# Kernel optimization log

Hardware: AMD Instinct MI355X
Metric: run time of the kernel (lower is better)

The kernel has to match this reference:

```python
import jax, jax.numpy as jnp
import numpy as np


def log_g(x):
    # log of g(x) = relu(x)+0.5 for x>=0, sigmoid(x) for x<0 (continuous minGRU activation)
    return jnp.where(x >= 0, jnp.log(jax.nn.relu(x) + 0.5), -jax.nn.softplus(-x))


def parallel_scan_log(log_coeffs, log_values):
    # log_coeffs: [B,T,H], log_values: [B,T+1,H]
    a_star = jnp.pad(jnp.cumsum(log_coeffs, axis=1), ((0, 0), (1, 0), (0, 0)))  # [B,T+1,H]
    log_h = a_star + jax.lax.cumlogsumexp(log_values - a_star, axis=1)
    return jnp.exp(log_h)  # [B,T+1,H]


def setup_inputs() -> dict:
    key = jax.random.key(0)
    B, T, D, H = 8, 4096, 1024, 1024
    k1, k2, k3, k4, k5, k6 = jax.random.split(key, 6)
    scale = 1.0 / np.sqrt(D)
    return {
        "x": jax.random.normal(k1, (B, T, D), dtype=jnp.float32),
        "h_0": jax.random.uniform(k2, (B, 1, H), dtype=jnp.float32),
        "W_z": jax.random.uniform(k3, (H, D), minval=-scale, maxval=scale, dtype=jnp.float32),
        "b_z": jax.random.uniform(k4, (H,), minval=-scale, maxval=scale, dtype=jnp.float32),
        "W_h": jax.random.uniform(k5, (H, D), minval=-scale, maxval=scale, dtype=jnp.float32),
        "b_h": jax.random.uniform(k6, (H,), minval=-scale, maxval=scale, dtype=jnp.float32),
    }


def reference(x, h_0, W_z, b_z, W_h, b_h):
    # k = linear_z(x)
    k = jnp.einsum('btd,hd->bth', x, W_z) + b_z                 # [B,T,H]
    log_z = -jax.nn.softplus(-k)                                # log sigmoid(k)
    log_coeffs = -jax.nn.softplus(k)                            # log (1 - sigmoid(k))
    log_h_0 = log_g(h_0)                                        # [B,1,H]
    log_tilde_h = log_g(jnp.einsum('btd,hd->bth', x, W_h) + b_h)  # [B,T,H]
    log_values = jnp.concatenate([log_h_0, log_z + log_tilde_h], axis=1)  # [B,T+1,H]
    h = parallel_scan_log(log_coeffs, log_values)               # [B,T+1,H]
    return h
```

## Files before the change

kernel.cpp:

```cpp
#include <hip/hip_runtime.h>
#include <stdint.h>

#define B_ 8
#define T_ 4096
#define D_ 1024
#define H_ 1024
#define M_ (B_*T_)
#define K_ D_
#define N_ H_
#define TC 32
#define NC (T_/TC)

typedef short short8 __attribute__((ext_vector_type(8)));
typedef float f32x4 __attribute__((ext_vector_type(4)));
typedef unsigned short ushort8v __attribute__((ext_vector_type(8)));

__device__ __forceinline__ float bf2f(unsigned short u) {
    union { unsigned int i; float f; } x; x.i = ((unsigned int)u) << 16; return x.f;
}
__device__ __forceinline__ unsigned short f2bf(float f) {
    union { float f; unsigned int i; } x; x.f = f;
    unsigned int u = x.i;
    unsigned int r = u + 0x7fffu + ((u >> 16) & 1u);
    return (unsigned short)(r >> 16);
}
__device__ __forceinline__ void gld_lds16(const unsigned short* g, unsigned short* l) {
    __builtin_amdgcn_global_load_lds(
        (const __attribute__((address_space(1))) void*)(const void*)g,
        (__attribute__((address_space(3))) void*)(void*)l, 16, 0, 0);
}
__device__ __forceinline__ float sigm_neg(float k) {
    return __builtin_amdgcn_rcpf(1.f + __expf(k));
}
__device__ __forceinline__ float gfun(float x) {
    float neg = __builtin_amdgcn_rcpf(1.f + __expf(-x));
    return x >= 0.f ? x + 0.5f : neg;
}

__global__ void cvt_kernel(const float* __restrict__ src, unsigned short* __restrict__ dst, int n4) {
    int i = blockIdx.x * blockDim.x + threadIdx.x;
    const int stride = gridDim.x * blockDim.x;
    for (; i < n4; i += stride) {
        float4 v = ((const float4*)src)[i];
        ushort4 o;
        o.x = f2bf(v.x); o.y = f2bf(v.y); o.z = f2bf(v.z); o.w = f2bf(v.w);
        ((ushort4*)dst)[i] = o;
    }
}

__global__ void cvtw_kernel(const float* __restrict__ Wz, const float* __restrict__ Wh,
                            unsigned short* __restrict__ wzb, unsigned short* __restrict__ whb, int n4) {
    const float* src = blockIdx.y ? Wh : Wz;
    unsigned short* dst = blockIdx.y ? whb : wzb;
    int i = blockIdx.x * blockDim.x + threadIdx.x;
    const int stride = gridDim.x * blockDim.x;
    for (; i < n4; i += stride) {
        float4 v = ((const float4*)src)[i];
        ushort4 o;
        o.x = f2bf(v.x); o.y = f2bf(v.y); o.z = f2bf(v.z); o.w = f2bf(v.w);
        ((ushort4*)dst)[i] = o;
    }
}

#define SB() __builtin_amdgcn_sched_barrier(0)
#define BAR() do { SB(); __builtin_amdgcn_s_barrier(); SB(); } while (0)

__global__ __launch_bounds__(512, 2) void gemm_kernel(
    const unsigned short* __restrict__ Xb,
    const unsigned short* __restrict__ Wzb,
    const unsigned short* __restrict__ Whb,
    const float* __restrict__ bz, const float* __restrict__ bh,
    unsigned short* __restrict__ KzOut, unsigned short* __restrict__ KhOut,
    int row_off)
{
    __shared__ __align__(16) unsigned short ldsA[2][256 * 64];
    __shared__ __align__(16) unsigned short ldsB[2][256 * 64];

    const int bx = blockIdx.x;
    const int bn = blockIdx.y;
    const int mat = blockIdx.z;
    const unsigned short* Wb = mat ? Whb : Wzb;
    const float* bias = mat ? bh : bz;
    unsigned short* Out = mat ? KhOut : KzOut;

    const int tid = threadIdx.x;
    const int w = tid >> 6, lane = tid & 63;
    const int wm = w >> 2, wn = w & 3;

    const int srow = lane >> 3;
    const int schunk = ((lane & 7) ^ srow) << 3;
    const unsigned short* gA = Xb + (size_t)(row_off + bx * 512 + srow) * K_ + schunk;
    const unsigned short* gB = Wb + (size_t)(bn * 256 + srow) * K_ + schunk;

#define STAGE_A(s, g, h) do { \
    gld_lds16(gA + (size_t)(((g) >> 4) * 256 + (h)*128 + w*8) * K_ + ((g)&15) * 64, \
              &ldsA[s][((h)*128 + w*8) * 64]); \
    gld_lds16(gA + (size_t)(((g) >> 4) * 256 + (h)*128 + 64 + w*8) * K_ + ((g)&15) * 64, \
              &ldsA[s][((h)*128 + 64 + w*8) * 64]); \
  } while (0)
#define STAGE_B(s, g, h) do { \
    gld_lds16(gB + (size_t)((h)*128 + w*8) * K_ + ((g)&15) * 64, \
              &ldsB[s][((h)*128 + w*8) * 64]); \
    gld_lds16(gB + (size_t)((h)*128 + 64 + w*8) * K_ + ((g)&15) * 64, \
              &ldsB[s][((h)*128 + 64 + w*8) * 64]); \
  } while (0)

    const int lrow = lane & 15;
    const int q = lane >> 4;
    const int sw0 = (q ^ (lane & 7)) << 3;

#define LDA(s, fm, kh) (*(const short8*)&ldsA[s][(wm*128 + (fm)*16 + lrow) * 64 + (sw0 ^ ((kh)*32))])
#define LDB(s, fn, kh) (*(const short8*)&ldsB[s][(wn*64  + (fn)*16 + lrow) * 64 + (sw0 ^ ((kh)*32))])

#define RD_A4(s, fmb) do { \
    _Pragma("unroll") for (int f = 0; f < 4; ++f) { Ar[f][0] = LDA(s, (fmb)+f, 0); Ar[f][1] = LDA(s, (fmb)+f, 1); } \
  } while (0)
#define RD_B2(s, fnb) do { \
    _Pragma("unroll") for (int g2_ = 0; g2_ < 2; ++g2_) { Br[(fnb)+g2_][0] = LDB(s, (fnb)+g2_, 0); Br[(fnb)+g2_][1] = LDB(s, (fnb)+g2_, 1); } \
  } while (0)

#define QUAD(mb, nb) do { \
    __builtin_amdgcn_s_setprio(1); \
    _Pragma("unroll") for (int f = 0; f < 4; ++f) { \
      _Pragma("unroll") for (int g2_ = 0; g2_ < 2; ++g2_) { \
        acc[(mb)+f][(nb)+g2_] = __builtin_amdgcn_mfma_f32_16x16x32_bf16(Ar[f][0], Br[(nb)+g2_][0], acc[(mb)+f][(nb)+g2_], 0, 0, 0); \
        acc[(mb)+f][(nb)+g2_] = __builtin_amdgcn_mfma_f32_16x16x32_bf16(Ar[f][1], Br[(nb)+g2_][1], acc[(mb)+f][(nb)+g2_], 0, 0, 0); \
      } \
    } \
    __builtin_amdgcn_s_setprio(0); \
  } while (0)

    f32x4 acc[8][4];
    short8 Ar[4][2], Br[4][2];

    float bb[4];
#pragma unroll
    for (int fn = 0; fn < 4; ++fn) bb[fn] = bias[bn * 256 + wn * 64 + fn * 16 + lrow];

    STAGE_B(0, 0, 0); STAGE_B(0, 0, 1);
    STAGE_A(0, 0, 0); STAGE_A(0, 0, 1);
    STAGE_B(1, 1, 0); STAGE_B(1, 1, 1);
    SB();
    asm volatile("s_waitcnt vmcnt(4)" ::: "memory");
    BAR();

#pragma unroll 1
    for (int t = 0; t < 2; ++t) {
#pragma unroll
        for (int i = 0; i < 8; ++i)
#pragma unroll
            for (int j = 0; j < 4; ++j) acc[i][j] = (f32x4){0.f, 0.f, 0.f, 0.f};

#pragma unroll 1
        for (int i = 0; i < 8; ++i) {
            const int g1 = t * 16 + 2 * i + 1;
            const int g2 = g1 + 1;
            const int g3 = g1 + 2;
            const bool st = (g2 < 32);

            RD_A4(0, 0); RD_B2(0, 0);
            STAGE_A(1, g1, 0);
            BAR();
            QUAD(0, 0);
            BAR();
            RD_B2(0, 2);
            STAGE_A(1, g1, 1);
            BAR();
            QUAD(0, 2);
            BAR();
            RD_A4(0, 4);
            if (st) STAGE_B(0, g2, 0);
            BAR();
            QUAD(4, 0);
            BAR();
            if (st) {
                STAGE_B(0, g2, 1);
                SB();
                asm volatile("s_waitcnt vmcnt(4)" ::: "memory");
            } else {
                asm volatile("s_waitcnt vmcnt(0)" ::: "memory");
            }
            BAR();
            QUAD(4, 2);
            BAR();
            RD_A4(1, 0); RD_B2(1, 0);
            if (st) STAGE_A(0, g2, 0);
            BAR();
            QUAD(0, 0);
            BAR();
            RD_B2(1, 2);
            if (st) STAGE_A(0, g2, 1);
            BAR();
            QUAD(0, 2);
            BAR();
            RD_A4(1, 4);
            if (st) STAGE_B(1, g3, 0);
            BAR();
            QUAD(4, 0);
            BAR();
            if (st) {
                STAGE_B(1, g3, 1);
                SB();
                asm volatile("s_waitcnt vmcnt(4)" ::: "memory");
            }
            BAR();
            QUAD(4, 2);
            BAR();
        }

#pragma unroll
        for (int fn = 0; fn < 4; ++fn) {
            const int n = bn * 256 + wn * 64 + fn * 16 + lrow;
#pragma unroll
            for (int fm = 0; fm < 8; ++fm) {
                const int mq = (row_off >> 2) + bx * 128 + t * 64 + wm * 32 + fm * 4 + q;
                ushort4 o;
                o.x = f2bf(acc[fm][fn][0] + bb[fn]);
                o.y = f2bf(acc[fm][fn][1] + bb[fn]);
                o.z = f2bf(acc[fm][fn][2] + bb[fn]);
                o.w = f2bf(acc[fm][fn][3] + bb[fn]);
                *(ushort4*)(Out + ((size_t)mq * N_ + n) * 4) = o;
            }
        }
    }
}


#define QUAD_MATH(Z0, Z1, HH0, HH1, CYSTMT)                                            \
    _Pragma("unroll")                                                                  \
    for (int r = 0; r < 4; r++) {                                                      \
        float kzf[4] = {bf2f(Z0[r]), bf2f(Z0[4 + r]), bf2f(Z1[r]), bf2f(Z1[4 + r])};   \
        float khf[4] = {bf2f(HH0[r]), bf2f(HH0[4 + r]), bf2f(HH1[r]), bf2f(HH1[4 + r])};\
        _Pragma("unroll")                                                              \
        for (int j = 0; j < 4; j++) {                                                  \
            float f = sigm_neg(kzf[j]);                           \
            float v = (1.f - f) * gfun(khf[j]);                 \
            CYSTMT                                                                     \
        }                                                                              \
    }

__global__ __launch_bounds__(256) void scanA_kernel(const unsigned short* __restrict__ Kz,
                                                    const unsigned short* __restrict__ Kh,
                                                    float* __restrict__ Fc, float* __restrict__ Vc)
{
    const int c = blockIdx.x, b = blockIdx.y;
    const int hb = threadIdx.x * 4;
    float F[4] = {1.f, 1.f, 1.f, 1.f}, V[4] = {0.f, 0.f, 0.f, 0.f};
    const size_t base0 = ((size_t)(b * (T_ / 4) + c * (TC / 4)) * N_ + hb) * 4;
    const size_t str = (size_t)N_ * 4;
    ushort8v cz0 = *(const ushort8v*)(Kz + base0);
    ushort8v cz1 = *(const ushort8v*)(Kz + base0 + 8);
    ushort8v ch0 = *(const ushort8v*)(Kh + base0);
    ushort8v ch1 = *(const ushort8v*)(Kh + base0 + 8);
    ushort8v az0 = *(const ushort8v*)(Kz + base0 + str);
    ushort8v az1 = *(const ushort8v*)(Kz + base0 + str + 8);
    ushort8v ah0 = *(const ushort8v*)(Kh + base0 + str);
    ushort8v ah1 = *(const ushort8v*)(Kh + base0 + str + 8);
#pragma unroll 1
    for (int qq = 0; qq < TC / 4; qq++) {
        const int qn = (qq + 2 < TC / 4) ? qq + 2 : TC / 4 - 1;
        const size_t nb = base0 + (size_t)qn * str;
        ushort8v bz0 = *(const ushort8v*)(Kz + nb);
        ushort8v bz1 = *(const ushort8v*)(Kz + nb + 8);
        ushort8v bh0 = *(const ushort8v*)(Kh + nb);
        ushort8v bh1 = *(const ushort8v*)(Kh + nb + 8);
        QUAD_MATH(cz0, cz1, ch0, ch1, { V[j] = f * V[j] + v; F[j] *= f; })
        cz0 = az0; cz1 = az1; ch0 = ah0; ch1 = ah1;
        az0 = bz0; az1 = bz1; ah0 = bh0; ah1 = bh1;
    }
    size_t o = ((size_t)(b * NC + c)) * H_ + hb;
    *(float4*)(Fc + o) = make_float4(F[0], F[1], F[2], F[3]);
    *(float4*)(Vc + o) = make_float4(V[0], V[1], V[2], V[3]);
}

__global__ __launch_bounds__(64) void scanB_kernel(const float* __restrict__ h0,
                                                   const float* __restrict__ Fc,
                                                   const float* __restrict__ Vc,
                                                   float* __restrict__ Carry,
                                                   float* __restrict__ Out)
{
    const int b = blockIdx.x;
    const int h = blockIdx.y * 256 + threadIdx.x * 4;
    float cy[4];
#pragma unroll
    for (int j = 0; j < 4; j++) cy[j] = gfun(h0[(size_t)b * H_ + h + j]);
    *(float4*)(Out + (size_t)b * (T_ + 1) * H_ + h) = make_float4(cy[0], cy[1], cy[2], cy[3]);
    size_t o = ((size_t)(b * NC)) * H_ + h;
    float4 F4 = *(const float4*)(Fc + o);
    float4 V4 = *(const float4*)(Vc + o);
    for (int c = 0; c < NC; c++) {
        const size_t on = o + H_;
        float4 nF, nV;
        if (c + 1 < NC) {
            nF = *(const float4*)(Fc + on);
            nV = *(const float4*)(Vc + on);
        }
        *(float4*)(Carry + o) = make_float4(cy[0], cy[1], cy[2], cy[3]);
        cy[0] = F4.x * cy[0] + V4.x;
        cy[1] = F4.y * cy[1] + V4.y;
        cy[2] = F4.z * cy[2] + V4.z;
        cy[3] = F4.w * cy[3] + V4.w;
        F4 = nF; V4 = nV; o = on;
    }
}

__global__ __launch_bounds__(256) void scanC_kernel(const unsigned short* __restrict__ Kz,
                                                    const unsigned short* __restrict__ Kh,
                                                    const float* __restrict__ Carry,
                                                    float* __restrict__ Out)
{
    const int c = blockIdx.x, b = blockIdx.y;
    const int hb = threadIdx.x * 4;
    float cy[4];
    {
        float4 c4 = *(const float4*)(Carry + ((size_t)(b * NC + c)) * H_ + hb);
        cy[0] = c4.x; cy[1] = c4.y; cy[2] = c4.z; cy[3] = c4.w;
    }
    const size_t base0 = ((size_t)(b * (T_ / 4) + c * (TC / 4)) * N_ + hb) * 4;
    const size_t str = (size_t)N_ * 4;
    size_t ob = ((size_t)(b * (T_ + 1) + c * TC + 1)) * H_ + hb;
    ushort8v cz0 = *(const ushort8v*)(Kz + base0);
    ushort8v cz1 = *(const ushort8v*)(Kz + base0 + 8);
    ushort8v ch0 = *(const ushort8v*)(Kh + base0);
    ushort8v ch1 = *(const ushort8v*)(Kh + base0 + 8);
    ushort8v az0 = *(const ushort8v*)(Kz + base0 + str);
    ushort8v az1 = *(const ushort8v*)(Kz + base0 + str + 8);
    ushort8v ah0 = *(const ushort8v*)(Kh + base0 + str);
    ushort8v ah1 = *(const ushort8v*)(Kh + base0 + str + 8);
#pragma unroll 1
    for (int qq = 0; qq < TC / 4; qq++) {
        const int qn = (qq + 2 < TC / 4) ? qq + 2 : TC / 4 - 1;
        const size_t nb = base0 + (size_t)qn * str;
        ushort8v bz0 = *(const ushort8v*)(Kz + nb);
        ushort8v bz1 = *(const ushort8v*)(Kz + nb + 8);
        ushort8v bh0 = *(const ushort8v*)(Kh + nb);
        ushort8v bh1 = *(const ushort8v*)(Kh + nb + 8);
        QUAD_MATH(cz0, cz1, ch0, ch1, {
            cy[j] = f * cy[j] + v;
            if (j == 3) { *(float4*)(Out + ob) = make_float4(cy[0], cy[1], cy[2], cy[3]); ob += H_; }
        })
        cz0 = az0; cz1 = az1; ch0 = ah0; ch1 = ah1;
        az0 = bz0; az1 = bz1; ah0 = bh0; ah1 = bh1;
    }
}

extern "C" void kernel_launch(void* const* d_in, const int* in_sizes, int n_in,
                              void* d_out, int out_size, void* d_ws, size_t ws_size,
                              hipStream_t stream)
{
    const float* x  = (const float*)d_in[0];
    const float* h0 = (const float*)d_in[1];
    const float* Wz = (const float*)d_in[2];
    const float* bz = (const float*)d_in[3];
    const float* Wh = (const float*)d_in[4];
    const float* bh = (const float*)d_in[5];
    float* out = (float*)d_out;

    char* ws = (char*)d_ws;
    unsigned short* xb  = (unsigned short*)ws; ws += (size_t)M_ * K_ * 2;
    unsigned short* wzb = (unsigned short*)ws; ws += (size_t)N_ * K_ * 2;
    unsigned short* whb = (unsigned short*)ws; ws += (size_t)N_ * K_ * 2;
    unsigned short* kz  = (unsigned short*)ws; ws += (size_t)M_ * N_ * 2;
    unsigned short* kh  = (unsigned short*)ws; ws += (size_t)M_ * N_ * 2;
    float* Fc    = (float*)ws; ws += (size_t)B_ * NC * H_ * 4;
    float* Vc    = (float*)ws; ws += (size_t)B_ * NC * H_ * 4;
    float* Carry = (float*)ws; ws += (size_t)B_ * NC * H_ * 4;

    cvt_kernel<<<2048, 256, 0, stream>>>(x, xb, M_ * K_ / 4);
    cvtw_kernel<<<dim3(128, 2), 256, 0, stream>>>(Wz, Wh, wzb, whb, N_ * K_ / 4);

    dim3 gg(32, 4, 2);
    gemm_kernel<<<gg, 512, 0, stream>>>(xb, wzb, whb, bz, bh, kz, kh, 0);
    gemm_kernel<<<gg, 512, 0, stream>>>(xb, wzb, whb, bz, bh, kz, kh, 16384);

    scanA_kernel<<<dim3(NC, B_), 256, 0, stream>>>(kz, kh, Fc, Vc);
    scanB_kernel<<<dim3(B_, H_ / 256), 64, 0, stream>>>(h0, Fc, Vc, Carry, out);
    scanC_kernel<<<dim3(NC, B_), 256, 0, stream>>>(kz, kh, Carry, out);
}
```

Measured before the change: 450.1 us.

## Merge GEMM launches and prefetch next A fragments during MFMA quads

Result: slower. 465.7 us (+3.5%).

```diff
diff --git a/kernel.cpp b/kernel.cpp
--- a/kernel.cpp
+++ b/kernel.cpp
@@ -70,8 +70,7 @@
     const unsigned short* __restrict__ Wzb,
     const unsigned short* __restrict__ Whb,
     const float* __restrict__ bz, const float* __restrict__ bh,
-    unsigned short* __restrict__ KzOut, unsigned short* __restrict__ KhOut,
-    int row_off)
+    unsigned short* __restrict__ KzOut, unsigned short* __restrict__ KhOut)
 {
     __shared__ __align__(16) unsigned short ldsA[2][256 * 64];
     __shared__ __align__(16) unsigned short ldsB[2][256 * 64];
@@ -89,7 +88,7 @@
 
     const int srow = lane >> 3;
     const int schunk = ((lane & 7) ^ srow) << 3;
-    const unsigned short* gA = Xb + (size_t)(row_off + bx * 512 + srow) * K_ + schunk;
+    const unsigned short* gA = Xb + (size_t)(bx * 1024 + srow) * K_ + schunk;
     const unsigned short* gB = Wb + (size_t)(bn * 256 + srow) * K_ + schunk;
 
 #define STAGE_A(s, g, h) do { \
@@ -112,26 +111,26 @@
 #define LDA(s, fm, kh) (*(const short8*)&ldsA[s][(wm*128 + (fm)*16 + lrow) * 64 + (sw0 ^ ((kh)*32))])
 #define LDB(s, fn, kh) (*(const short8*)&ldsB[s][(wn*64  + (fn)*16 + lrow) * 64 + (sw0 ^ ((kh)*32))])
 
-#define RD_A4(s, fmb) do { \
-    _Pragma("unroll") for (int f = 0; f < 4; ++f) { Ar[f][0] = LDA(s, (fmb)+f, 0); Ar[f][1] = LDA(s, (fmb)+f, 1); } \
+#define RD_A4(DST, s, fmb) do { \
+    _Pragma("unroll") for (int f = 0; f < 4; ++f) { DST[f][0] = LDA(s, (fmb)+f, 0); DST[f][1] = LDA(s, (fmb)+f, 1); } \
   } while (0)
 #define RD_B2(s, fnb) do { \
     _Pragma("unroll") for (int g2_ = 0; g2_ < 2; ++g2_) { Br[(fnb)+g2_][0] = LDB(s, (fnb)+g2_, 0); Br[(fnb)+g2_][1] = LDB(s, (fnb)+g2_, 1); } \
   } while (0)
 
-#define QUAD(mb, nb) do { \
+#define QUAD(AF, mb, nb) do { \
     __builtin_amdgcn_s_setprio(1); \
     _Pragma("unroll") for (int f = 0; f < 4; ++f) { \
       _Pragma("unroll") for (int g2_ = 0; g2_ < 2; ++g2_) { \
-        acc[(mb)+f][(nb)+g2_] = __builtin_amdgcn_mfma_f32_16x16x32_bf16(Ar[f][0], Br[(nb)+g2_][0], acc[(mb)+f][(nb)+g2_], 0, 0, 0); \
-        acc[(mb)+f][(nb)+g2_] = __builtin_amdgcn_mfma_f32_16x16x32_bf16(Ar[f][1], Br[(nb)+g2_][1], acc[(mb)+f][(nb)+g2_], 0, 0, 0); \
+        acc[(mb)+f][(nb)+g2_] = __builtin_amdgcn_mfma_f32_16x16x32_bf16(AF[f][0], Br[(nb)+g2_][0], acc[(mb)+f][(nb)+g2_], 0, 0, 0); \
+        acc[(mb)+f][(nb)+g2_] = __builtin_amdgcn_mfma_f32_16x16x32_bf16(AF[f][1], Br[(nb)+g2_][1], acc[(mb)+f][(nb)+g2_], 0, 0, 0); \
       } \
     } \
     __builtin_amdgcn_s_setprio(0); \
   } while (0)
 
     f32x4 acc[8][4];
-    short8 Ar[4][2], Br[4][2];
+    short8 Ar[4][2], Ar2[4][2], Br[4][2];
 
     float bb[4];
 #pragma unroll
@@ -143,9 +142,10 @@
     SB();
     asm volatile("s_waitcnt vmcnt(4)" ::: "memory");
     BAR();
+    RD_A4(Ar2, 0, 0); RD_B2(0, 0);
 
 #pragma unroll 1
-    for (int t = 0; t < 2; ++t) {
+    for (int t = 0; t < 4; ++t) {
 #pragma unroll
         for (int i = 0; i < 8; ++i)
 #pragma unroll
@@ -156,22 +156,23 @@
             const int g1 = t * 16 + 2 * i + 1;
             const int g2 = g1 + 1;
             const int g3 = g1 + 2;
-            const bool st = (g2 < 32);
-
-            RD_A4(0, 0); RD_B2(0, 0);
+            const bool st = (g2 < 64);
+
             STAGE_A(1, g1, 0);
             BAR();
-            QUAD(0, 0);
-            BAR();
             RD_B2(0, 2);
+            SB();
+            QUAD(Ar2, 0, 0);
+            BAR();
             STAGE_A(1, g1, 1);
             BAR();
-            QUAD(0, 2);
-            BAR();
-            RD_A4(0, 4);
+            RD_A4(Ar, 0, 4);
+            SB();
+            QUAD(Ar2, 0, 2);
+            BAR();
             if (st) STAGE_B(0, g2, 0);
             BAR();
-            QUAD(4, 0);
+            QUAD(Ar, 4, 0);
             BAR();
             if (st) {
                 STAGE_B(0, g2, 1);
@@ -181,22 +182,25 @@
                 asm volatile("s_waitcnt vmcnt(0)" ::: "memory");
             }
             BAR();
-            QUAD(4, 2);
-            BAR();
-            RD_A4(1, 0); RD_B2(1, 0);
+            RD_A4(Ar2, 1, 0); RD_B2(1, 0);
+            SB();
+            QUAD(Ar, 4, 2);
+            BAR();
             if (st) STAGE_A(0, g2, 0);
             BAR();
-            QUAD(0, 0);
-            BAR();
             RD_B2(1, 2);
+            SB();
+            QUAD(Ar2, 0, 0);
+            BAR();
             if (st) STAGE_A(0, g2, 1);
             BAR();
-            QUAD(0, 2);
-            BAR();
-            RD_A4(1, 4);
+            RD_A4(Ar, 1, 4);
+            SB();
+            QUAD(Ar2, 0, 2);
+            BAR();
             if (st) STAGE_B(1, g3, 0);
             BAR();
-            QUAD(4, 0);
+            QUAD(Ar, 4, 0);
             BAR();
             if (st) {
                 STAGE_B(1, g3, 1);
@@ -204,7 +208,8 @@
                 asm volatile("s_waitcnt vmcnt(4)" ::: "memory");
             }
             BAR();
-            QUAD(4, 2);
+            if (st) { RD_A4(Ar2, 0, 0); RD_B2(0, 0); SB(); }
+            QUAD(Ar, 4, 2);
             BAR();
         }
 
@@ -213,7 +218,7 @@
             const int n = bn * 256 + wn * 64 + fn * 16 + lrow;
 #pragma unroll
             for (int fm = 0; fm < 8; ++fm) {
-                const int mq = (row_off >> 2) + bx * 128 + t * 64 + wm * 32 + fm * 4 + q;
+                const int mq = (bx * 4 + t) * 64 + wm * 32 + fm * 4 + q;
                 ushort4 o;
                 o.x = f2bf(acc[fm][fn][0] + bb[fn]);
                 o.y = f2bf(acc[fm][fn][1] + bb[fn]);
@@ -369,9 +374,8 @@
     cvt_kernel<<<2048, 256, 0, stream>>>(x, xb, M_ * K_ / 4);
     cvtw_kernel<<<dim3(128, 2), 256, 0, stream>>>(Wz, Wh, wzb, whb, N_ * K_ / 4);
 
-    dim3 gg(32, 4, 2);
-    gemm_kernel<<<gg, 512, 0, stream>>>(xb, wzb, whb, bz, bh, kz, kh, 0);
-    gemm_kernel<<<gg, 512, 0, stream>>>(xb, wzb, whb, bz, bh, kz, kh, 16384);
+    dim3 gg(M_ / 1024, N_ / 256, 2);
+    gemm_kernel<<<gg, 512, 0, stream>>>(xb, wzb, whb, bz, bh, kz, kh);
 
     scanA_kernel<<<dim3(NC, B_), 256, 0, stream>>>(kz, kh, Fc, Vc);
     scanB_kernel<<<dim3(B_, H_ / 256), 64, 0, stream>>>(h0, Fc, Vc, Carry, out);
```
